# Performance work log

Measured on AMD Instinct MI355X. Metric: run time of the kernel, lower is better.

The kernel has to match this reference:

```python
import jax, jax.numpy as jnp
import numpy as np

D_MODEL = 768
D_STATE = 8
EXPAND = 2
D_HEAD = 64
D_CONV = 4
D_INNER = EXPAND * D_MODEL            # 1536
N_HEADS = D_INNER // D_HEAD           # 24
PARAM_DIM = 2                         # (A_freq, dt) per head per step
D_PROJ = 2 * D_INNER + N_HEADS * PARAM_DIM  # 3120
D_FF = 4 * D_MODEL
BATCH, SEQ = 2, 2048


def setup_inputs() -> dict:
    key = jax.random.key(0)
    ks = jax.random.split(key, 8)
    def s(k, shape, scale):
        return jax.random.normal(k, shape, dtype=jnp.float32) * scale
    return {
        "x": s(ks[0], (BATCH, SEQ, D_MODEL), 1.0),
        "norm1_w": jnp.ones((D_MODEL,), jnp.float32),
        "w_in": s(ks[1], (D_MODEL, D_PROJ), D_MODEL ** -0.5),
        "conv_w": s(ks[2], (D_INNER, D_CONV), D_CONV ** -0.5),
        "w_bc": s(ks[3], (D_INNER, 2 * N_HEADS * D_STATE), D_INNER ** -0.5),
        "D_skip": s(ks[4], (N_HEADS,), 1.0),
        "w_out": s(ks[5], (D_INNER, D_MODEL), D_INNER ** -0.5),
        "norm2_w": jnp.ones((D_MODEL,), jnp.float32),
        "ff_w1": s(ks[6], (D_MODEL, D_FF), D_MODEL ** -0.5),
        "ff_b1": jnp.zeros((D_FF,), jnp.float32),
        "ff_w2": s(ks[7], (D_FF, D_MODEL), D_FF ** -0.5),
        "ff_b2": jnp.zeros((D_MODEL,), jnp.float32),
    }


def _rmsnorm(x, w, eps=1e-6):
    return x * jax.lax.rsqrt(jnp.mean(x * x, axis=-1, keepdims=True) + eps) * w


def _l2norm(x, eps=1e-12):
    # normalize_bc=True: L2-normalize B/C rows over the state dim
    return x * jax.lax.rsqrt(jnp.sum(x * x, axis=-1, keepdims=True) + eps)


def _mixer(x, w_in, conv_w, w_bc, D_skip, w_out):
    Bsz, T, _ = x.shape
    proj = x @ w_in  # (B,T,3120)
    gate, vraw, params = jnp.split(proj, [D_INNER, 2 * D_INNER], axis=-1)
    # causal depthwise conv over time
    vpad = jnp.pad(vraw, ((0, 0), (D_CONV - 1, 0), (0, 0)))
    kernel = conv_w.T[:, None, :]  # (K, 1, C) for WIO, groups=C
    conv = jax.lax.conv_general_dilated(
        vpad, kernel, window_strides=(1,), padding='VALID',
        dimension_numbers=('NWC', 'WIO', 'NWC'), feature_group_count=D_INNER)
    v = jax.nn.silu(conv)  # (B,T,D_INNER)
    # B/C projections per head (normalized rows)
    bc = (v @ w_bc).reshape(Bsz, T, N_HEADS, 2, D_STATE)
    Bm = _l2norm(bc[..., 0, :])  # (B,T,H,N)
    Cm = _l2norm(bc[..., 1, :])  # (B,T,H,N)
    # LinOSS-IM discretizer: per-head time-varying frequency A and step dt
    p = params.reshape(Bsz, T, N_HEADS, PARAM_DIM)
    A = jax.nn.softplus(p[..., 0])
    dt = jax.nn.sigmoid(p[..., 1])
    S = 1.0 / (1.0 + dt * dt * A)  # implicit-midpoint Schur factor
    u = v.reshape(Bsz, T, N_HEADS, D_HEAD)
    tfirst = lambda a: jnp.moveaxis(a, 1, 0)

    def step(carry, inp):
        z, xs = carry  # each (B,H,N,P): velocity / position of the oscillator
        Bt, Ct, At, dtt, St, ut = inp
        d = dtt[..., None, None]
        a = At[..., None, None]
        s = St[..., None, None]
        bu = Bt[..., :, None] * ut[..., None, :]  # (B,H,N,P)
        z = s * (z - d * a * xs + d * bu)
        xs = xs + d * z
        y = jnp.einsum('bhn,bhnp->bhp', Ct, xs)
        return (z, xs), y

    z0 = jnp.zeros((Bsz, N_HEADS, D_STATE, D_HEAD), x.dtype)
    _, ys = jax.lax.scan(step, (z0, z0),
                         (tfirst(Bm), tfirst(Cm), tfirst(A), tfirst(dt), tfirst(S), tfirst(u)))
    y = jnp.moveaxis(ys, 0, 1)  # (B,T,H,P)
    # gate + per-head skip (D * u), then out projection
    gated = (y + D_skip[None, None, :, None] * u) * jax.nn.silu(gate).reshape(Bsz, T, N_HEADS, D_HEAD)
    return gated.reshape(Bsz, T, D_INNER) @ w_out


def reference(x, norm1_w, w_in, conv_w, w_bc, D_skip, w_out, norm2_w, ff_w1, ff_b1, ff_w2, ff_b2):
    x = x + _mixer(_rmsnorm(x, norm1_w), w_in, conv_w, w_bc, D_skip, w_out)
    h = _rmsnorm(x, norm2_w)
    return x + (jax.nn.gelu(h @ ff_w1 + ff_b1) @ ff_w2 + ff_b2)
```

## Files before the change

### kernel.cpp

```cpp
#include <hip/hip_runtime.h>

#define DMODEL 768
#define DINNER 1536
#define NHEADS 24
#define DHEAD  64
#define DSTATE 8
#define DPROJ  3120
#define DFF    3072
#define BATCH  2
#define SEQ    2048
#define BTTOT  (BATCH*SEQ)
#define NCHUNK 64
#define CT     32

typedef unsigned short u16;
typedef __attribute__((ext_vector_type(8))) short bf16x8;
typedef __attribute__((ext_vector_type(4))) float f32x4;

__device__ __forceinline__ float b2f(u16 u){
  union { unsigned u; float f; } x; x.u = ((unsigned)u) << 16; return x.f;
}
__device__ __forceinline__ u16 f2b(float f){
  union { float f; unsigned u; } x; x.f = f;
  unsigned r = x.u + 0x7FFF + ((x.u >> 16) & 1);
  return (u16)(r >> 16);
}
__device__ __forceinline__ float ldin(const void* p, size_t i, bool f32){
  return f32 ? ((const float*)p)[i] : b2f(((const u16*)p)[i]);
}
__device__ __forceinline__ bool wire_f32(const u16* probe){ return probe[0] == 0; }

__global__ __launch_bounds__(256) void transpose_to_bf16(
    const void* __restrict__ src, u16* __restrict__ dst, int R, int C,
    const u16* __restrict__ probe)
{
  const bool f32 = wire_f32(probe);
  __shared__ u16 tile[32][33];
  const int tx = threadIdx.x & 31, ty = threadIdx.x >> 5;
  const int c0 = blockIdx.x * 32, r0 = blockIdx.y * 32;
  #pragma unroll
  for (int i = 0; i < 32; i += 8){
    int r = r0 + ty + i, c = c0 + tx;
    u16 val = 0;
    if (r < R && c < C){
      size_t idx = (size_t)r * C + c;
      val = f32 ? f2b(((const float*)src)[idx]) : ((const u16*)src)[idx];
    }
    tile[ty + i][tx] = val;
  }
  __syncthreads();
  #pragma unroll
  for (int i = 0; i < 32; i += 8){
    int c = c0 + ty + i, r = r0 + tx;
    if (c < C && r < R) dst[(size_t)c * R + r] = tile[tx][ty + i];
  }
}

template <bool XWIRE>
__global__ __launch_bounds__(256) void rmsnorm_k(
    const void* __restrict__ x, const void* __restrict__ w, u16* __restrict__ out,
    const u16* __restrict__ probe)
{
  const bool f32 = wire_f32(probe);
  const size_t row = blockIdx.x;
  float v[3]; float s = 0.f;
  #pragma unroll
  for (int i = 0; i < 3; i++){
    size_t idx = row * DMODEL + threadIdx.x + 256 * i;
    float f = XWIRE ? ldin(x, idx, f32) : ((const float*)x)[idx];
    v[i] = f; s += f * f;
  }
  #pragma unroll
  for (int o = 32; o > 0; o >>= 1) s += __shfl_xor(s, o);
  __shared__ float red[4];
  if ((threadIdx.x & 63) == 0) red[threadIdx.x >> 6] = s;
  __syncthreads();
  float tot = red[0] + red[1] + red[2] + red[3];
  float inv = rsqrtf(tot * (1.0f / DMODEL) + 1e-6f);
  #pragma unroll
  for (int i = 0; i < 3; i++){
    int c = threadIdx.x + 256 * i;
    out[row * DMODEL + c] = f2b(v[i] * inv * ldin(w, c, f32));
  }
}

template <class Epi>
__global__ __launch_bounds__(256, 2) void gemm_bt(
    const u16* __restrict__ A, const u16* __restrict__ Bt,
    int M, int N, int Ks, int ldK, Epi epi, const u16* __restrict__ probe)
{
  const bool wf32 = wire_f32(probe);
  __shared__ __align__(16) u16 As[128 * 64];
  __shared__ __align__(16) u16 Bs[128 * 64];
  const int tid  = threadIdx.x;
  const int lane = tid & 63;
  const int wave = tid >> 6;
  const int wm = (wave >> 1) * 64;
  const int wn = (wave & 1) * 64;
  const int m0 = blockIdx.y * 128;
  const int n0 = blockIdx.x * 128;
  const int z  = blockIdx.z;
  const int kbase = z * Ks;
  const int rt = tid >> 3;
  const int cb = (tid & 7) * 8;
  const int sw = (rt & 7) * 8;

  f32x4 acc[4][4];
  const f32x4 z4 = {0.f, 0.f, 0.f, 0.f};
  #pragma unroll
  for (int i = 0; i < 4; i++)
    #pragma unroll
    for (int j = 0; j < 4; j++) acc[i][j] = z4;

  const int krow = lane & 15;
  const int kqo  = (lane >> 4) * 8;
  const int rsw  = (krow & 7) * 8;

  for (int k0 = kbase; k0 < kbase + Ks; k0 += 64){
    __syncthreads();
    #pragma unroll
    for (int i = 0; i < 4; i++){
      const u16* ga = A + ((size_t)(m0 + rt + 32 * i) * ldK + k0 + (cb ^ sw));
      __builtin_amdgcn_global_load_lds(
          (const __attribute__((address_space(1))) unsigned*)ga,
          (__attribute__((address_space(3))) unsigned*)(As + i * 2048 + wave * 512),
          16, 0, 0);
      int rb = n0 + rt + 32 * i; if (rb > N - 1) rb = N - 1;
      const u16* gb = Bt + ((size_t)rb * ldK + k0 + (cb ^ sw));
      __builtin_amdgcn_global_load_lds(
          (const __attribute__((address_space(1))) unsigned*)gb,
          (__attribute__((address_space(3))) unsigned*)(Bs + i * 2048 + wave * 512),
          16, 0, 0);
    }
    __syncthreads();
    #pragma unroll
    for (int ks = 0; ks < 2; ks++){
      const int koff = (ks * 32 + kqo) ^ rsw;
      bf16x8 af[4], bfr[4];
      #pragma unroll
      for (int i = 0; i < 4; i++){
        af[i]  = *(const bf16x8*)(As + (wm + i * 16 + krow) * 64 + koff);
        bfr[i] = *(const bf16x8*)(Bs + (wn + i * 16 + krow) * 64 + koff);
      }
      #pragma unroll
      for (int i = 0; i < 4; i++)
        #pragma unroll
        for (int j = 0; j < 4; j++)
          acc[i][j] = __builtin_amdgcn_mfma_f32_16x16x32_bf16(af[i], bfr[j], acc[i][j], 0, 0, 0);
    }
  }

  const int mb = m0 + wm + (lane >> 4) * 4;
  const int nb = n0 + wn + (lane & 15);
  #pragma unroll
  for (int i = 0; i < 4; i++)
    #pragma unroll
    for (int j = 0; j < 4; j++)
      #pragma unroll
      for (int r = 0; r < 4; r++){
        int m = mb + i * 16 + r;
        int n = nb + j * 16;
        if (n < N) epi(acc[i][j][r], m, n, wf32, z);
      }
}

struct EpiF32 {
  float* out; int ldo;
  __device__ void operator()(float v, int m, int n, bool, int) const {
    out[(size_t)m * ldo + n] = v;
  }
};
struct EpiPart {
  float* out; size_t ss; int ldo;
  __device__ void operator()(float v, int m, int n, bool, int z) const {
    out[(size_t)z * ss + (size_t)m * ldo + n] = v;
  }
};
struct EpiBiasGelu {
  u16* out; const void* bias; int ldo;
  __device__ void operator()(float v, int m, int n, bool f32, int) const {
    float x = v + ldin(bias, n, f32);
    float t = 0.7978845608028654f * (x + 0.044715f * x * x * x);
    out[(size_t)m * ldo + n] = f2b(0.5f * x * (1.0f + tanhf(t)));
  }
};

__global__ __launch_bounds__(256) void reduceW_k(
    const float* __restrict__ pW, const void* __restrict__ x, float* __restrict__ x2,
    const u16* __restrict__ probe)
{
  const bool f32 = wire_f32(probe);
  const size_t MN = (size_t)BTTOT * DMODEL;
  size_t i = ((size_t)blockIdx.x * 256 + threadIdx.x) * 4;
  float4 a = *(const float4*)(pW + i);
  float4 b = *(const float4*)(pW + MN + i);
  float4 o;
  o.x = a.x + b.x + ldin(x, i + 0, f32);
  o.y = a.y + b.y + ldin(x, i + 1, f32);
  o.z = a.z + b.z + ldin(x, i + 2, f32);
  o.w = a.w + b.w + ldin(x, i + 3, f32);
  *(float4*)(x2 + i) = o;
}

__global__ __launch_bounds__(256) void reduceF_k(
    const float* __restrict__ pF, const void* __restrict__ bias,
    const float* __restrict__ x2, void* __restrict__ out,
    const u16* __restrict__ probe)
{
  const bool f32 = wire_f32(probe);
  const size_t MN = (size_t)BTTOT * DMODEL;
  size_t i = ((size_t)blockIdx.x * 256 + threadIdx.x) * 4;
  int n = (int)(i % DMODEL);
  float4 a = *(const float4*)(pF + i);
  float4 b = *(const float4*)(pF + MN + i);
  float4 c = *(const float4*)(pF + 2 * MN + i);
  float4 d = *(const float4*)(pF + 3 * MN + i);
  float4 r = *(const float4*)(x2 + i);
  float o0 = a.x + b.x + c.x + d.x + r.x + ldin(bias, n + 0, f32);
  float o1 = a.y + b.y + c.y + d.y + r.y + ldin(bias, n + 1, f32);
  float o2 = a.z + b.z + c.z + d.z + r.z + ldin(bias, n + 2, f32);
  float o3 = a.w + b.w + c.w + d.w + r.w + ldin(bias, n + 3, f32);
  if (f32){
    *(float4*)((float*)out + i) = make_float4(o0, o1, o2, o3);
  } else {
    u16* po = (u16*)out + i;
    po[0] = f2b(o0); po[1] = f2b(o1); po[2] = f2b(o2); po[3] = f2b(o3);
  }
}

__global__ __launch_bounds__(256) void conv_silu_k(
    const float* __restrict__ proj, const void* __restrict__ cw, u16* __restrict__ v,
    const u16* __restrict__ probe)
{
  const bool f32 = wire_f32(probe);
  int idx = blockIdx.x * 256 + threadIdx.x;
  int c = idx % DINNER; int bt = idx / DINNER;
  if (bt >= BTTOT) return;
  int t = bt & (SEQ - 1);
  float w0 = ldin(cw, c * 4 + 0, f32), w1 = ldin(cw, c * 4 + 1, f32);
  float w2 = ldin(cw, c * 4 + 2, f32), w3 = ldin(cw, c * 4 + 3, f32);
  const float* pc = proj + (size_t)bt * DPROJ + DINNER + c;
  float acc = w3 * pc[0];
  if (t >= 1) acc = fmaf(w2, pc[-DPROJ], acc);
  if (t >= 2) acc = fmaf(w1, pc[-2 * DPROJ], acc);
  if (t >= 3) acc = fmaf(w0, pc[-3 * DPROJ], acc);
  float out = acc / (1.f + __expf(-acc));
  v[(size_t)bt * DINNER + c] = f2b(out);
}

__global__ __launch_bounds__(256) void prep_k(
    const float* __restrict__ proj, const float* __restrict__ pB,
    float* __restrict__ bcn, float* __restrict__ prm)
{
  const size_t MN = (size_t)BTTOT * 2 * NHEADS * DSTATE;
  int idx = blockIdx.x * 256 + threadIdx.x;
  if (idx >= BTTOT * NHEADS) return;
  int h = idx % NHEADS; int bt = idx / NHEADS;
  int b = bt >> 11, t = bt & (SEQ - 1);
  float p0 = proj[(size_t)bt * DPROJ + 2 * DINNER + h * 2];
  float p1 = proj[(size_t)bt * DPROJ + 2 * DINNER + h * 2 + 1];
  float A  = fmaxf(p0, 0.f) + log1pf(__expf(-fabsf(p0)));
  float dt = 1.f / (1.f + __expf(-p1));
  float S  = 1.f / (1.f + dt * dt * A);
  size_t pb = ((size_t)(b * NHEADS + h) * SEQ + t);
  float* pr = prm + pb * 4;
  pr[0] = S * dt * A; pr[1] = dt; pr[2] = S * dt; pr[3] = S;
  const float* br = pB + (size_t)bt * (2 * NHEADS * DSTATE) + h * 16;
  float Bv[8], Cv[8]; float sB = 1e-12f, sC = 1e-12f;
  #pragma unroll
  for (int j = 0; j < 8; j++){
    Bv[j] = br[j] + br[MN + j] + br[2 * MN + j] + br[3 * MN + j];
    sB += Bv[j] * Bv[j];
  }
  #pragma unroll
  for (int j = 0; j < 8; j++){
    Cv[j] = br[8 + j] + br[MN + 8 + j] + br[2 * MN + 8 + j] + br[3 * MN + 8 + j];
    sC += Cv[j] * Cv[j];
  }
  float rB = rsqrtf(sB), rC = rsqrtf(sC);
  float* o = bcn + pb * 16;
  #pragma unroll
  for (int j = 0; j < 8; j++){ o[j * 2] = Bv[j] * rB; o[j * 2 + 1] = Cv[j] * rC; }
}


__global__ __launch_bounds__(256) void scanP(
    const float* __restrict__ prm, float4* __restrict__ phiE)
{
  int g = blockIdx.x * 256 + threadIdx.x;
  if (g >= 48 * NCHUNK) return;
  const float4* pr = (const float4*)(prm + (size_t)g * CT * 4);
  float p00 = 1.f, p01 = 0.f, p10 = 0.f, p11 = 1.f;
  #pragma unroll 4
  for (int t = 0; t < CT; t++){
    float4 pv = pr[t];
    float n00 = pv.w * p00 - pv.x * p10;
    float n01 = pv.w * p01 - pv.x * p11;
    float n10 = fmaf(pv.z, p00, pv.w * p10);
    float n11 = fmaf(pv.z, p01, pv.w * p11);
    p00 = n00; p01 = n01; p10 = n10; p11 = n11;
  }
  phiE[g] = make_float4(p00, p01, p10, p11);
}

__global__ __launch_bounds__(256) void scanA(
    const float* __restrict__ bcn, const float* __restrict__ prm,
    const u16* __restrict__ v, float2* __restrict__ rend)
{
  const int g = blockIdx.x * 4 + (threadIdx.x >> 6);
  const int bh = g >> 6, chunk = g & 63;
  const int b = bh / NHEADS, h = bh % NHEADS;
  const int t0 = chunk * CT;
  const int lane = threadIdx.x & 63;
  const float4* bcB = (const float4*)(bcn + ((size_t)bh * SEQ + t0) * 16);
  const float4* prB = (const float4*)(prm + ((size_t)bh * SEQ + t0) * 4);
  const u16* vB = v + ((size_t)b * SEQ + t0) * DINNER + h * DHEAD + lane;

  float z[8], xs[8];
  #pragma unroll
  for (int n = 0; n < 8; n++){ z[n] = 0.f; xs[n] = 0.f; }
  #pragma unroll 4
  for (int t = 0; t < CT; t++){
    float4 pv  = prB[t];
    float4 bc0 = bcB[t * 4 + 0], bc1 = bcB[t * 4 + 1];
    float4 bc2 = bcB[t * 4 + 2], bc3 = bcB[t * 4 + 3];
    float u = b2f(vB[(size_t)t * DINNER]);
    float Bv[8] = {bc0.x, bc0.z, bc1.x, bc1.z, bc2.x, bc2.z, bc3.x, bc3.z};
    #pragma unroll
    for (int n = 0; n < 8; n++){
      z[n]  = pv.w * z[n] - pv.x * xs[n] + pv.z * (Bv[n] * u);
      xs[n] = fmaf(pv.y, z[n], xs[n]);
    }
  }
  float2* rb = rend + (size_t)g * 512 + lane;
  #pragma unroll
  for (int n = 0; n < 8; n++) rb[n * 64] = make_float2(z[n], xs[n]);
}

__global__ __launch_bounds__(512) void scanB(
    const float2* __restrict__ rend, const float4* __restrict__ phiE,
    float2* __restrict__ s0)
{
  const int bh = blockIdx.x, tid = threadIdx.x;
  float z = 0.f, xs = 0.f;
  for (int c = 0; c < NCHUNK; c++){
    size_t idx = ((size_t)bh * NCHUNK + c) * 512 + tid;
    s0[idx] = make_float2(z, xs);
    float4 ph = phiE[bh * NCHUNK + c];
    float2 r  = rend[idx];
    float nz = ph.x * z + ph.y * xs + r.x;
    float nx = ph.z * z + ph.w * xs + r.y;
    z = nz; xs = nx;
  }
}

__global__ __launch_bounds__(256) void scanC(
    const float* __restrict__ bcn, const float* __restrict__ prm,
    const u16* __restrict__ v, const float* __restrict__ proj,
    const float2* __restrict__ s0, const void* __restrict__ Dsk,
    u16* __restrict__ gated, const u16* __restrict__ probe)
{
  const bool f32 = wire_f32(probe);
  const int g = blockIdx.x * 4 + (threadIdx.x >> 6);
  const int bh = g >> 6, chunk = g & 63;
  const int b = bh / NHEADS, h = bh % NHEADS;
  const int t0 = chunk * CT;
  const int lane = threadIdx.x & 63;
  const float4* bcB = (const float4*)(bcn + ((size_t)bh * SEQ + t0) * 16);
  const float4* prB = (const float4*)(prm + ((size_t)bh * SEQ + t0) * 4);
  const u16*   vB = v     + ((size_t)b * SEQ + t0) * DINNER + h * DHEAD + lane;
  const float* gB = proj  + ((size_t)b * SEQ + t0) * DPROJ  + h * DHEAD + lane;
  u16*         oB = gated + ((size_t)b * SEQ + t0) * DINNER + h * DHEAD + lane;
  const float dsk = ldin(Dsk, h, f32);

  float z[8], xs[8];
  const float2* sb = s0 + (size_t)g * 512 + lane;
  #pragma unroll
  for (int n = 0; n < 8; n++){ float2 s = sb[n * 64]; z[n] = s.x; xs[n] = s.y; }
  #pragma unroll 4
  for (int t = 0; t < CT; t++){
    float4 pv  = prB[t];
    float4 bc0 = bcB[t * 4 + 0], bc1 = bcB[t * 4 + 1];
    float4 bc2 = bcB[t * 4 + 2], bc3 = bcB[t * 4 + 3];
    float u  = b2f(vB[(size_t)t * DINNER]);
    float gt = gB[(size_t)t * DPROJ];
    float Bv[8] = {bc0.x, bc0.z, bc1.x, bc1.z, bc2.x, bc2.z, bc3.x, bc3.z};
    float Cv[8] = {bc0.y, bc0.w, bc1.y, bc1.w, bc2.y, bc2.w, bc3.y, bc3.w};
    float y = 0.f;
    #pragma unroll
    for (int n = 0; n < 8; n++){
      z[n]  = pv.w * z[n] - pv.x * xs[n] + pv.z * (Bv[n] * u);
      xs[n] = fmaf(pv.y, z[n], xs[n]);
      y     = fmaf(Cv[n], xs[n], y);
    }
    float sil = gt / (1.f + __expf(-gt));
    oB[(size_t)t * DINNER] = f2b((y + dsk * u) * sil);
  }
}

extern "C" void kernel_launch(void* const* d_in, const int* in_sizes, int n_in,
                              void* d_out, int out_size, void* d_ws, size_t ws_size,
                              hipStream_t stream)
{
  const void* x      = d_in[0];
  const u16*  probe  = (const u16*)d_in[1];
  const void* norm1w = d_in[1];
  const void* w_in   = d_in[2];
  const void* conv_w = d_in[3];
  const void* w_bc   = d_in[4];
  const void* Dsk    = d_in[5];
  const void* w_out  = d_in[6];
  const void* norm2w = d_in[7];
  const void* ff_w1  = d_in[8];
  const void* ff_b1  = d_in[9];
  const void* ff_w2  = d_in[10];
  const void* ff_b2  = d_in[11];

  char* wsb = (char*)d_ws;
  size_t off = 0;
  auto alloc = [&](size_t bytes) -> void* {
    void* p = wsb + off; off += (bytes + 255) & ~(size_t)255; return p;
  };
  u16*   w_inT  = (u16*)  alloc((size_t)DPROJ * DMODEL * 2);
  u16*   w_bcT  = (u16*)  alloc((size_t)(2 * NHEADS * DSTATE) * DINNER * 2);
  u16*   w_outT = (u16*)  alloc((size_t)DMODEL * DINNER * 2);
  u16*   ff_w1T = (u16*)  alloc((size_t)DFF * DMODEL * 2);
  u16*   ff_w2T = (u16*)  alloc((size_t)DMODEL * DFF * 2);
  u16*   xn     = (u16*)  alloc((size_t)BTTOT * DMODEL * 2);
  float* proj   = (float*)alloc((size_t)BTTOT * DPROJ * 4);
  u16*   v      = (u16*)  alloc((size_t)BTTOT * DINNER * 2);
  float* bcn    = (float*)alloc((size_t)48 * SEQ * 16 * 4);
  float* prm    = (float*)alloc((size_t)48 * SEQ * 4 * 4);
  u16*   gated  = (u16*)  alloc((size_t)BTTOT * DINNER * 2);
  float* x2     = (float*)alloc((size_t)BTTOT * DMODEL * 4);
  u16*   hbuf   = (u16*)  alloc((size_t)BTTOT * DMODEL * 2);
  float4* phiE  = (float4*)alloc((size_t)48 * NCHUNK * 16);
  char*  scrU   = (char*) alloc((size_t)4 * BTTOT * DMODEL * 4);
  float* pB     = (float*)scrU;
  float2* rend  = (float2*)scrU;
  float2* s0b   = (float2*)(scrU + (size_t)48 * NCHUNK * 512 * 8);
  float* pF     = (float*)scrU;
  u16*   a1     = (u16*)proj;
  float* pW     = (float*)((char*)proj + (size_t)BTTOT * DFF * 2);

  transpose_to_bf16<<<dim3(98, 24), 256, 0, stream>>>(w_in,  w_inT,  DMODEL, DPROJ, probe);
  transpose_to_bf16<<<dim3(12, 48), 256, 0, stream>>>(w_bc,  w_bcT,  DINNER, 2 * NHEADS * DSTATE, probe);
  transpose_to_bf16<<<dim3(24, 48), 256, 0, stream>>>(w_out, w_outT, DINNER, DMODEL, probe);
  transpose_to_bf16<<<dim3(96, 24), 256, 0, stream>>>(ff_w1, ff_w1T, DMODEL, DFF, probe);
  transpose_to_bf16<<<dim3(24, 96), 256, 0, stream>>>(ff_w2, ff_w2T, DFF, DMODEL, probe);

  rmsnorm_k<true><<<BTTOT, 256, 0, stream>>>(x, norm1w, xn, probe);

  gemm_bt<<<dim3(25, 32, 1), 256, 0, stream>>>(xn, w_inT, BTTOT, DPROJ, DMODEL, DMODEL,
                                               EpiF32{proj, DPROJ}, probe);
  conv_silu_k<<<(BTTOT * DINNER) / 256, 256, 0, stream>>>(proj, conv_w, v, probe);
  gemm_bt<<<dim3(3, 32, 4), 256, 0, stream>>>(v, w_bcT, BTTOT, 2 * NHEADS * DSTATE,
                                              1536 / 4, DINNER,
                                              EpiPart{pB, (size_t)BTTOT * 2 * NHEADS * DSTATE, 2 * NHEADS * DSTATE}, probe);
  prep_k<<<(BTTOT * NHEADS) / 256, 256, 0, stream>>>(proj, pB, bcn, prm);

  scanP<<<12, 256, 0, stream>>>(prm, phiE);
  scanA<<<48 * NCHUNK / 4, 256, 0, stream>>>(bcn, prm, v, rend);
  scanB<<<48, 512, 0, stream>>>(rend, phiE, s0b);
  scanC<<<48 * NCHUNK / 4, 256, 0, stream>>>(bcn, prm, v, proj, s0b, Dsk, gated, probe);

  gemm_bt<<<dim3(6, 32, 2), 256, 0, stream>>>(gated, w_outT, BTTOT, DMODEL, 1536 / 2, DINNER,
                                              EpiPart{pW, (size_t)BTTOT * DMODEL, DMODEL}, probe);
  reduceW_k<<<(BTTOT * DMODEL) / 1024, 256, 0, stream>>>(pW, x, x2, probe);
  rmsnorm_k<false><<<BTTOT, 256, 0, stream>>>(x2, norm2w, hbuf, probe);
  gemm_bt<<<dim3(24, 32, 1), 256, 0, stream>>>(hbuf, ff_w1T, BTTOT, DFF, DMODEL, DMODEL,
                                               EpiBiasGelu{a1, ff_b1, DFF}, probe);
  gemm_bt<<<dim3(6, 32, 4), 256, 0, stream>>>(a1, ff_w2T, BTTOT, DMODEL, 3072 / 4, DFF,
                                              EpiPart{pF, (size_t)BTTOT * DMODEL, DMODEL}, probe);
  reduceF_k<<<(BTTOT * DMODEL) / 1024, 256, 0, stream>>>(pF, ff_b2, x2, d_out, probe);
}
```

Before: 415.5 us.

## Store intermediates in bf16, merge transposes, fuse residual reduce into rmsnorm

Switches the projection output and the split-K partial buffers from fp32 to bf16, which roughly halves their memory traffic. The five weight transposes are merged into one launch, the reduceW kernel is fused into the second rmsnorm, conv_silu is vectorised four channels per thread, and the split-K factor is raised for two GEMMs. Rounding split-K partials and the projection to bf16 adds precision loss.

Measured after the change: 394.4 us. 5.1% less time.

```diff
diff --git a/kernel.cpp b/kernel.cpp
--- a/kernel.cpp
+++ b/kernel.cpp
@@ -30,21 +30,30 @@
 }
 __device__ __forceinline__ bool wire_f32(const u16* probe){ return probe[0] == 0; }
 
-__global__ __launch_bounds__(256) void transpose_to_bf16(
-    const void* __restrict__ src, u16* __restrict__ dst, int R, int C,
-    const u16* __restrict__ probe)
+struct TDesc { const void* src; u16* dst; int R, C, bx, blk0; };
+struct TPack { TDesc d[5]; };
+
+__global__ __launch_bounds__(256) void transpose5_k(TPack P, const u16* __restrict__ probe)
 {
   const bool f32 = wire_f32(probe);
+  int bk = blockIdx.x;
+  int s = 0;
+  #pragma unroll
+  for (int i = 1; i < 5; i++) if (bk >= P.d[i].blk0) s = i;
+  const TDesc D = P.d[s];
+  const int local = bk - D.blk0;
+  const int cx = local % D.bx, ry = local / D.bx;
+  const int c0 = cx * 32, r0 = ry * 32;
+  const int R = D.R, C = D.C;
   __shared__ u16 tile[32][33];
   const int tx = threadIdx.x & 31, ty = threadIdx.x >> 5;
-  const int c0 = blockIdx.x * 32, r0 = blockIdx.y * 32;
   #pragma unroll
   for (int i = 0; i < 32; i += 8){
     int r = r0 + ty + i, c = c0 + tx;
     u16 val = 0;
     if (r < R && c < C){
       size_t idx = (size_t)r * C + c;
-      val = f32 ? f2b(((const float*)src)[idx]) : ((const u16*)src)[idx];
+      val = f32 ? f2b(((const float*)D.src)[idx]) : ((const u16*)D.src)[idx];
     }
     tile[ty + i][tx] = val;
   }
@@ -52,11 +61,10 @@
   #pragma unroll
   for (int i = 0; i < 32; i += 8){
     int c = c0 + ty + i, r = r0 + tx;
-    if (c < C && r < R) dst[(size_t)c * R + r] = tile[tx][ty + i];
-  }
-}
-
-template <bool XWIRE>
+    if (c < C && r < R) D.dst[(size_t)c * R + r] = tile[tx][ty + i];
+  }
+}
+
 __global__ __launch_bounds__(256) void rmsnorm_k(
     const void* __restrict__ x, const void* __restrict__ w, u16* __restrict__ out,
     const u16* __restrict__ probe)
@@ -67,7 +75,37 @@
   #pragma unroll
   for (int i = 0; i < 3; i++){
     size_t idx = row * DMODEL + threadIdx.x + 256 * i;
-    float f = XWIRE ? ldin(x, idx, f32) : ((const float*)x)[idx];
+    float f = ldin(x, idx, f32);
+    v[i] = f; s += f * f;
+  }
+  #pragma unroll
+  for (int o = 32; o > 0; o >>= 1) s += __shfl_xor(s, o);
+  __shared__ float red[4];
+  if ((threadIdx.x & 63) == 0) red[threadIdx.x >> 6] = s;
+  __syncthreads();
+  float tot = red[0] + red[1] + red[2] + red[3];
+  float inv = rsqrtf(tot * (1.0f / DMODEL) + 1e-6f);
+  #pragma unroll
+  for (int i = 0; i < 3; i++){
+    int c = threadIdx.x + 256 * i;
+    out[row * DMODEL + c] = f2b(v[i] * inv * ldin(w, c, f32));
+  }
+}
+
+__global__ __launch_bounds__(256) void rmsnormW_k(
+    const u16* __restrict__ pW, const void* __restrict__ x, const void* __restrict__ w,
+    float* __restrict__ x2, u16* __restrict__ out, const u16* __restrict__ probe)
+{
+  const bool f32 = wire_f32(probe);
+  const size_t row = blockIdx.x;
+  const size_t MN = (size_t)BTTOT * DMODEL;
+  float v[3]; float s = 0.f;
+  #pragma unroll
+  for (int i = 0; i < 3; i++){
+    size_t idx = row * DMODEL + threadIdx.x + 256 * i;
+    float f = ldin(x, idx, f32) + b2f(pW[idx]) + b2f(pW[MN + idx])
+            + b2f(pW[2 * MN + idx]) + b2f(pW[3 * MN + idx]);
+    x2[idx] = f;
     v[i] = f; s += f * f;
   }
   #pragma unroll
@@ -164,16 +202,16 @@
       }
 }
 
-struct EpiF32 {
-  float* out; int ldo;
+struct EpiBf16 {
+  u16* out; int ldo;
   __device__ void operator()(float v, int m, int n, bool, int) const {
-    out[(size_t)m * ldo + n] = v;
+    out[(size_t)m * ldo + n] = f2b(v);
   }
 };
-struct EpiPart {
-  float* out; size_t ss; int ldo;
+struct EpiPartB {
+  u16* out; size_t ss; int ldo;
   __device__ void operator()(float v, int m, int n, bool, int z) const {
-    out[(size_t)z * ss + (size_t)m * ldo + n] = v;
+    out[(size_t)z * ss + (size_t)m * ldo + n] = f2b(v);
   }
 };
 struct EpiBiasGelu {
@@ -185,25 +223,8 @@
   }
 };
 
-__global__ __launch_bounds__(256) void reduceW_k(
-    const float* __restrict__ pW, const void* __restrict__ x, float* __restrict__ x2,
-    const u16* __restrict__ probe)
-{
-  const bool f32 = wire_f32(probe);
-  const size_t MN = (size_t)BTTOT * DMODEL;
-  size_t i = ((size_t)blockIdx.x * 256 + threadIdx.x) * 4;
-  float4 a = *(const float4*)(pW + i);
-  float4 b = *(const float4*)(pW + MN + i);
-  float4 o;
-  o.x = a.x + b.x + ldin(x, i + 0, f32);
-  o.y = a.y + b.y + ldin(x, i + 1, f32);
-  o.z = a.z + b.z + ldin(x, i + 2, f32);
-  o.w = a.w + b.w + ldin(x, i + 3, f32);
-  *(float4*)(x2 + i) = o;
-}
-
 __global__ __launch_bounds__(256) void reduceF_k(
-    const float* __restrict__ pF, const void* __restrict__ bias,
+    const u16* __restrict__ pF, const void* __restrict__ bias,
     const float* __restrict__ x2, void* __restrict__ out,
     const u16* __restrict__ probe)
 {
@@ -211,78 +232,97 @@
   const size_t MN = (size_t)BTTOT * DMODEL;
   size_t i = ((size_t)blockIdx.x * 256 + threadIdx.x) * 4;
   int n = (int)(i % DMODEL);
-  float4 a = *(const float4*)(pF + i);
-  float4 b = *(const float4*)(pF + MN + i);
-  float4 c = *(const float4*)(pF + 2 * MN + i);
-  float4 d = *(const float4*)(pF + 3 * MN + i);
   float4 r = *(const float4*)(x2 + i);
-  float o0 = a.x + b.x + c.x + d.x + r.x + ldin(bias, n + 0, f32);
-  float o1 = a.y + b.y + c.y + d.y + r.y + ldin(bias, n + 1, f32);
-  float o2 = a.z + b.z + c.z + d.z + r.z + ldin(bias, n + 2, f32);
-  float o3 = a.w + b.w + c.w + d.w + r.w + ldin(bias, n + 3, f32);
+  float o[4] = {r.x, r.y, r.z, r.w};
+  #pragma unroll
+  for (int k = 0; k < 4; k++){
+    ushort4 p = *(const ushort4*)(pF + k * MN + i);
+    o[0] += b2f(p.x); o[1] += b2f(p.y); o[2] += b2f(p.z); o[3] += b2f(p.w);
+  }
+  #pragma unroll
+  for (int j = 0; j < 4; j++) o[j] += ldin(bias, n + j, f32);
   if (f32){
-    *(float4*)((float*)out + i) = make_float4(o0, o1, o2, o3);
+    *(float4*)((float*)out + i) = make_float4(o[0], o[1], o[2], o[3]);
   } else {
     u16* po = (u16*)out + i;
-    po[0] = f2b(o0); po[1] = f2b(o1); po[2] = f2b(o2); po[3] = f2b(o3);
+    po[0] = f2b(o[0]); po[1] = f2b(o[1]); po[2] = f2b(o[2]); po[3] = f2b(o[3]);
   }
 }
 
 __global__ __launch_bounds__(256) void conv_silu_k(
-    const float* __restrict__ proj, const void* __restrict__ cw, u16* __restrict__ v,
+    const u16* __restrict__ proj, const void* __restrict__ cw, u16* __restrict__ v,
     const u16* __restrict__ probe)
 {
   const bool f32 = wire_f32(probe);
   int idx = blockIdx.x * 256 + threadIdx.x;
-  int c = idx % DINNER; int bt = idx / DINNER;
-  if (bt >= BTTOT) return;
+  int c4 = (idx % (DINNER / 4)) * 4;
+  int bt = idx / (DINNER / 4);
   int t = bt & (SEQ - 1);
-  float w0 = ldin(cw, c * 4 + 0, f32), w1 = ldin(cw, c * 4 + 1, f32);
-  float w2 = ldin(cw, c * 4 + 2, f32), w3 = ldin(cw, c * 4 + 3, f32);
-  const float* pc = proj + (size_t)bt * DPROJ + DINNER + c;
-  float acc = w3 * pc[0];
-  if (t >= 1) acc = fmaf(w2, pc[-DPROJ], acc);
-  if (t >= 2) acc = fmaf(w1, pc[-2 * DPROJ], acc);
-  if (t >= 3) acc = fmaf(w0, pc[-3 * DPROJ], acc);
-  float out = acc / (1.f + __expf(-acc));
-  v[(size_t)bt * DINNER + c] = f2b(out);
+  const u16* base = proj + (size_t)bt * DPROJ + DINNER + c4;
+  float acc[4];
+  {
+    ushort4 p = *(const ushort4*)base;
+    acc[0] = ldin(cw, (c4 + 0) * 4 + 3, f32) * b2f(p.x);
+    acc[1] = ldin(cw, (c4 + 1) * 4 + 3, f32) * b2f(p.y);
+    acc[2] = ldin(cw, (c4 + 2) * 4 + 3, f32) * b2f(p.z);
+    acc[3] = ldin(cw, (c4 + 3) * 4 + 3, f32) * b2f(p.w);
+  }
+  #pragma unroll
+  for (int j = 1; j <= 3; j++){
+    if (t >= j){
+      ushort4 p = *(const ushort4*)(base - j * DPROJ);
+      acc[0] = fmaf(ldin(cw, (c4 + 0) * 4 + 3 - j, f32), b2f(p.x), acc[0]);
+      acc[1] = fmaf(ldin(cw, (c4 + 1) * 4 + 3 - j, f32), b2f(p.y), acc[1]);
+      acc[2] = fmaf(ldin(cw, (c4 + 2) * 4 + 3 - j, f32), b2f(p.z), acc[2]);
+      acc[3] = fmaf(ldin(cw, (c4 + 3) * 4 + 3 - j, f32), b2f(p.w), acc[3]);
+    }
+  }
+  ushort4 o;
+  o.x = f2b(acc[0] / (1.f + __expf(-acc[0])));
+  o.y = f2b(acc[1] / (1.f + __expf(-acc[1])));
+  o.z = f2b(acc[2] / (1.f + __expf(-acc[2])));
+  o.w = f2b(acc[3] / (1.f + __expf(-acc[3])));
+  *(ushort4*)(v + (size_t)bt * DINNER + c4) = o;
 }
 
 __global__ __launch_bounds__(256) void prep_k(
-    const float* __restrict__ proj, const float* __restrict__ pB,
+    const u16* __restrict__ proj, const u16* __restrict__ pB,
     float* __restrict__ bcn, float* __restrict__ prm)
 {
-  const size_t MN = (size_t)BTTOT * 2 * NHEADS * DSTATE;
+  const size_t MNb = (size_t)BTTOT * 2 * NHEADS * DSTATE;
   int idx = blockIdx.x * 256 + threadIdx.x;
   if (idx >= BTTOT * NHEADS) return;
   int h = idx % NHEADS; int bt = idx / NHEADS;
   int b = bt >> 11, t = bt & (SEQ - 1);
-  float p0 = proj[(size_t)bt * DPROJ + 2 * DINNER + h * 2];
-  float p1 = proj[(size_t)bt * DPROJ + 2 * DINNER + h * 2 + 1];
+  float p0 = b2f(proj[(size_t)bt * DPROJ + 2 * DINNER + h * 2]);
+  float p1 = b2f(proj[(size_t)bt * DPROJ + 2 * DINNER + h * 2 + 1]);
   float A  = fmaxf(p0, 0.f) + log1pf(__expf(-fabsf(p0)));
   float dt = 1.f / (1.f + __expf(-p1));
   float S  = 1.f / (1.f + dt * dt * A);
   size_t pb = ((size_t)(b * NHEADS + h) * SEQ + t);
   float* pr = prm + pb * 4;
   pr[0] = S * dt * A; pr[1] = dt; pr[2] = S * dt; pr[3] = S;
-  const float* br = pB + (size_t)bt * (2 * NHEADS * DSTATE) + h * 16;
-  float Bv[8], Cv[8]; float sB = 1e-12f, sC = 1e-12f;
-  #pragma unroll
-  for (int j = 0; j < 8; j++){
-    Bv[j] = br[j] + br[MN + j] + br[2 * MN + j] + br[3 * MN + j];
-    sB += Bv[j] * Bv[j];
-  }
-  #pragma unroll
-  for (int j = 0; j < 8; j++){
-    Cv[j] = br[8 + j] + br[MN + 8 + j] + br[2 * MN + 8 + j] + br[3 * MN + 8 + j];
-    sC += Cv[j] * Cv[j];
-  }
+  const u16* br = pB + (size_t)bt * (2 * NHEADS * DSTATE) + h * 16;
+  float Bv[8] = {0,0,0,0,0,0,0,0}, Cv[8] = {0,0,0,0,0,0,0,0};
+  #pragma unroll
+  for (int k = 0; k < 8; k++){
+    ushort4 b0 = *(const ushort4*)(br + k * MNb);
+    ushort4 b1 = *(const ushort4*)(br + k * MNb + 4);
+    ushort4 c0 = *(const ushort4*)(br + k * MNb + 8);
+    ushort4 c1 = *(const ushort4*)(br + k * MNb + 12);
+    Bv[0] += b2f(b0.x); Bv[1] += b2f(b0.y); Bv[2] += b2f(b0.z); Bv[3] += b2f(b0.w);
+    Bv[4] += b2f(b1.x); Bv[5] += b2f(b1.y); Bv[6] += b2f(b1.z); Bv[7] += b2f(b1.w);
+    Cv[0] += b2f(c0.x); Cv[1] += b2f(c0.y); Cv[2] += b2f(c0.z); Cv[3] += b2f(c0.w);
+    Cv[4] += b2f(c1.x); Cv[5] += b2f(c1.y); Cv[6] += b2f(c1.z); Cv[7] += b2f(c1.w);
+  }
+  float sB = 1e-12f, sC = 1e-12f;
+  #pragma unroll
+  for (int j = 0; j < 8; j++){ sB += Bv[j] * Bv[j]; sC += Cv[j] * Cv[j]; }
   float rB = rsqrtf(sB), rC = rsqrtf(sC);
   float* o = bcn + pb * 16;
   #pragma unroll
   for (int j = 0; j < 8; j++){ o[j * 2] = Bv[j] * rB; o[j * 2 + 1] = Cv[j] * rC; }
 }
-
 
 __global__ __launch_bounds__(256) void scanP(
     const float* __restrict__ prm, float4* __restrict__ phiE)
@@ -356,7 +396,7 @@
 
 __global__ __launch_bounds__(256) void scanC(
     const float* __restrict__ bcn, const float* __restrict__ prm,
-    const u16* __restrict__ v, const float* __restrict__ proj,
+    const u16* __restrict__ v, const u16* __restrict__ proj,
     const float2* __restrict__ s0, const void* __restrict__ Dsk,
     u16* __restrict__ gated, const u16* __restrict__ probe)
 {
@@ -368,9 +408,9 @@
   const int lane = threadIdx.x & 63;
   const float4* bcB = (const float4*)(bcn + ((size_t)bh * SEQ + t0) * 16);
   const float4* prB = (const float4*)(prm + ((size_t)bh * SEQ + t0) * 4);
-  const u16*   vB = v     + ((size_t)b * SEQ + t0) * DINNER + h * DHEAD + lane;
-  const float* gB = proj  + ((size_t)b * SEQ + t0) * DPROJ  + h * DHEAD + lane;
-  u16*         oB = gated + ((size_t)b * SEQ + t0) * DINNER + h * DHEAD + lane;
+  const u16* vB = v     + ((size_t)b * SEQ + t0) * DINNER + h * DHEAD + lane;
+  const u16* gB = proj  + ((size_t)b * SEQ + t0) * DPROJ  + h * DHEAD + lane;
+  u16*       oB = gated + ((size_t)b * SEQ + t0) * DINNER + h * DHEAD + lane;
   const float dsk = ldin(Dsk, h, f32);
 
   float z[8], xs[8];
@@ -383,7 +423,7 @@
     float4 bc0 = bcB[t * 4 + 0], bc1 = bcB[t * 4 + 1];
     float4 bc2 = bcB[t * 4 + 2], bc3 = bcB[t * 4 + 3];
     float u  = b2f(vB[(size_t)t * DINNER]);
-    float gt = gB[(size_t)t * DPROJ];
+    float gt = b2f(gB[(size_t)t * DPROJ]);
     float Bv[8] = {bc0.x, bc0.z, bc1.x, bc1.z, bc2.x, bc2.z, bc3.x, bc3.z};
     float Cv[8] = {bc0.y, bc0.w, bc1.y, bc1.w, bc2.y, bc2.w, bc3.y, bc3.w};
     float y = 0.f;
@@ -427,7 +467,7 @@
   u16*   ff_w1T = (u16*)  alloc((size_t)DFF * DMODEL * 2);
   u16*   ff_w2T = (u16*)  alloc((size_t)DMODEL * DFF * 2);
   u16*   xn     = (u16*)  alloc((size_t)BTTOT * DMODEL * 2);
-  float* proj   = (float*)alloc((size_t)BTTOT * DPROJ * 4);
+  u16*   proj   = (u16*)  alloc((size_t)BTTOT * DPROJ * 2);
   u16*   v      = (u16*)  alloc((size_t)BTTOT * DINNER * 2);
   float* bcn    = (float*)alloc((size_t)48 * SEQ * 16 * 4);
   float* prm    = (float*)alloc((size_t)48 * SEQ * 4 * 4);
@@ -435,28 +475,30 @@
   float* x2     = (float*)alloc((size_t)BTTOT * DMODEL * 4);
   u16*   hbuf   = (u16*)  alloc((size_t)BTTOT * DMODEL * 2);
   float4* phiE  = (float4*)alloc((size_t)48 * NCHUNK * 16);
-  char*  scrU   = (char*) alloc((size_t)4 * BTTOT * DMODEL * 4);
-  float* pB     = (float*)scrU;
+  char*  scrU   = (char*) alloc((size_t)27 * 1024 * 1024);
+  u16*   pB     = (u16*)scrU;
   float2* rend  = (float2*)scrU;
   float2* s0b   = (float2*)(scrU + (size_t)48 * NCHUNK * 512 * 8);
-  float* pF     = (float*)scrU;
-  u16*   a1     = (u16*)proj;
-  float* pW     = (float*)((char*)proj + (size_t)BTTOT * DFF * 2);
-
-  transpose_to_bf16<<<dim3(98, 24), 256, 0, stream>>>(w_in,  w_inT,  DMODEL, DPROJ, probe);
-  transpose_to_bf16<<<dim3(12, 48), 256, 0, stream>>>(w_bc,  w_bcT,  DINNER, 2 * NHEADS * DSTATE, probe);
-  transpose_to_bf16<<<dim3(24, 48), 256, 0, stream>>>(w_out, w_outT, DINNER, DMODEL, probe);
-  transpose_to_bf16<<<dim3(96, 24), 256, 0, stream>>>(ff_w1, ff_w1T, DMODEL, DFF, probe);
-  transpose_to_bf16<<<dim3(24, 96), 256, 0, stream>>>(ff_w2, ff_w2T, DFF, DMODEL, probe);
-
-  rmsnorm_k<true><<<BTTOT, 256, 0, stream>>>(x, norm1w, xn, probe);
+  u16*   pF     = (u16*)scrU;
+  u16*   pW     = proj;
+  u16*   a1     = proj;
+
+  TPack tp;
+  tp.d[0] = {w_in,  w_inT,  DMODEL, DPROJ,               98, 0};
+  tp.d[1] = {w_bc,  w_bcT,  DINNER, 2 * NHEADS * DSTATE, 12, 2352};
+  tp.d[2] = {w_out, w_outT, DINNER, DMODEL,              24, 2928};
+  tp.d[3] = {ff_w1, ff_w1T, DMODEL, DFF,                 96, 4080};
+  tp.d[4] = {ff_w2, ff_w2T, DFF,    DMODEL,              24, 6384};
+  transpose5_k<<<8688, 256, 0, stream>>>(tp, probe);
+
+  rmsnorm_k<<<BTTOT, 256, 0, stream>>>(x, norm1w, xn, probe);
 
   gemm_bt<<<dim3(25, 32, 1), 256, 0, stream>>>(xn, w_inT, BTTOT, DPROJ, DMODEL, DMODEL,
-                                               EpiF32{proj, DPROJ}, probe);
-  conv_silu_k<<<(BTTOT * DINNER) / 256, 256, 0, stream>>>(proj, conv_w, v, probe);
-  gemm_bt<<<dim3(3, 32, 4), 256, 0, stream>>>(v, w_bcT, BTTOT, 2 * NHEADS * DSTATE,
-                                              1536 / 4, DINNER,
-                                              EpiPart{pB, (size_t)BTTOT * 2 * NHEADS * DSTATE, 2 * NHEADS * DSTATE}, probe);
+                                               EpiBf16{proj, DPROJ}, probe);
+  conv_silu_k<<<(BTTOT * DINNER) / 1024, 256, 0, stream>>>(proj, conv_w, v, probe);
+  gemm_bt<<<dim3(3, 32, 8), 256, 0, stream>>>(v, w_bcT, BTTOT, 2 * NHEADS * DSTATE,
+                                              1536 / 8, DINNER,
+                                              EpiPartB{pB, (size_t)BTTOT * 2 * NHEADS * DSTATE, 2 * NHEADS * DSTATE}, probe);
   prep_k<<<(BTTOT * NHEADS) / 256, 256, 0, stream>>>(proj, pB, bcn, prm);
 
   scanP<<<12, 256, 0, stream>>>(prm, phiE);
@@ -464,13 +506,12 @@
   scanB<<<48, 512, 0, stream>>>(rend, phiE, s0b);
   scanC<<<48 * NCHUNK / 4, 256, 0, stream>>>(bcn, prm, v, proj, s0b, Dsk, gated, probe);
 
-  gemm_bt<<<dim3(6, 32, 2), 256, 0, stream>>>(gated, w_outT, BTTOT, DMODEL, 1536 / 2, DINNER,
-                                              EpiPart{pW, (size_t)BTTOT * DMODEL, DMODEL}, probe);
-  reduceW_k<<<(BTTOT * DMODEL) / 1024, 256, 0, stream>>>(pW, x, x2, probe);
-  rmsnorm_k<false><<<BTTOT, 256, 0, stream>>>(x2, norm2w, hbuf, probe);
+  gemm_bt<<<dim3(6, 32, 4), 256, 0, stream>>>(gated, w_outT, BTTOT, DMODEL, 1536 / 4, DINNER,
+                                              EpiPartB{pW, (size_t)BTTOT * DMODEL, DMODEL}, probe);
+  rmsnormW_k<<<BTTOT, 256, 0, stream>>>(pW, x, norm2w, x2, hbuf, probe);
   gemm_bt<<<dim3(24, 32, 1), 256, 0, stream>>>(hbuf, ff_w1T, BTTOT, DFF, DMODEL, DMODEL,
                                                EpiBiasGelu{a1, ff_b1, DFF}, probe);
   gemm_bt<<<dim3(6, 32, 4), 256, 0, stream>>>(a1, ff_w2T, BTTOT, DMODEL, 3072 / 4, DFF,
-                                              EpiPart{pF, (size_t)BTTOT * DMODEL, DMODEL}, probe);
+                                              EpiPartB{pF, (size_t)BTTOT * DMODEL, DMODEL}, probe);
   reduceF_k<<<(BTTOT * DMODEL) / 1024, 256, 0, stream>>>(pF, ff_b2, x2, d_out, probe);
 }
```
